# Optimization experiments

Measured on AMD Instinct MI355X. Metric: run time of the kernel, lower is better.

The kernel has to match this reference:

```python
import jax, jax.numpy as jnp
import numpy as np

N = 1024          # number of nodes
E = 32768         # number of edges
S = 4             # num_scales
STEPS = 31        # num_steps
MIN_SIGMA = 0.1
MAX_SIGMA = 3.0
EPS = 1e-12       # F.normalize eps


def setup_inputs() -> dict:
    key = jax.random.key(0)
    k1, k2 = jax.random.split(key, 2)
    coords = jax.random.normal(k1, (N, 3), dtype=jnp.float32)
    edge_index = jax.random.randint(k2, (2, E), 0, N, dtype=jnp.int64)
    # learned parameter, initialized exactly as in the module
    log_sigmas = jnp.linspace(jnp.log(jnp.float32(MIN_SIGMA)),
                              jnp.log(jnp.float32(MAX_SIGMA)), S).astype(jnp.float32)
    return {"coords": coords, "log_sigmas": log_sigmas, "edge_index": edge_index}


def reference(coords, log_sigmas, edge_index):
    n = coords.shape[0]
    # pairwise squared euclidean distances (cdist(..)^2)  [N,N]
    diff = coords[:, None, :] - coords[None, :, :]
    d2 = jnp.sum(diff * diff, axis=-1)

    sigmas = jnp.sort(jnp.exp(log_sigmas))                       # [S]
    w = jnp.exp(-d2[None, :, :] / (2.0 * sigmas[:, None, None] ** 2))  # [S,N,N]
    eye = jnp.eye(n, dtype=w.dtype)
    w = w * (1.0 - eye)                                          # zero diagonal
    row_sum = jnp.sum(w, axis=2, keepdims=True)                  # L1 row norm (w>=0)
    P = w / jnp.maximum(row_sum, EPS)                            # row-stochastic, 0 rows -> 0

    ei, ej = edge_index[0], edge_index[1]

    def step(P_k, _):
        P_k = P_k @ P                                            # batched [S,N,N] GEMM
        diag = jnp.diagonal(P_k, axis1=1, axis2=2)               # [S,N]
        edge = P_k[:, ei, ej]                                    # [S,E]
        return P_k, (diag, edge)

    P0 = jnp.broadcast_to(eye, P.shape)
    _, (diags, edges) = jax.lax.scan(step, P0, None, length=STEPS)
    # diags: [STEPS,S,N] -> node features [N, S*STEPS] (scale-major, step-minor)
    node_features = jnp.transpose(diags, (2, 1, 0)).reshape(n, S * STEPS)
    edge_features = jnp.transpose(edges, (2, 1, 0)).reshape(ei.shape[0], S * STEPS)
    return node_features, edge_features
```

## Files before the change

### kernel.cpp

```cpp
#include <hip/hip_runtime.h>

#define N 1024
#define NE 32768
#define S 4
#define STEPS 31
#define FEAT (S * STEPS)
#define PLANE ((size_t)S * N * N)
#define MAXT 192

typedef short short8 __attribute__((ext_vector_type(8)));
typedef short short4v __attribute__((ext_vector_type(4)));
typedef float f32x4 __attribute__((ext_vector_type(4)));
typedef int int4v __attribute__((ext_vector_type(4)));

__device__ __forceinline__ ushort f2bf(float x) {
    union { float f; unsigned u; } v; v.f = x;
    unsigned r = v.u + 0x7fffu + ((v.u >> 16) & 1u);
    return (ushort)(r >> 16);
}
__device__ __forceinline__ float bf2f(ushort h) {
    union { unsigned u; float f; } v; v.u = ((unsigned)h) << 16;
    return v.f;
}

__device__ __forceinline__ void gload16(const ushort* g, ushort* l) {
    __builtin_amdgcn_global_load_lds(
        (const __attribute__((address_space(1))) unsigned int*)g,
        (__attribute__((address_space(3))) unsigned int*)l, 16, 0, 0);
}

__global__ __launch_bounds__(256) void build_P(const float* __restrict__ coords,
                                               const float* __restrict__ log_sigmas,
                                               ushort* __restrict__ Oh,
                                               ushort* __restrict__ Ol)
{
    const int i   = blockIdx.x;
    const int tid = threadIdx.x;

    float sg[S];
#pragma unroll
    for (int s = 0; s < S; ++s) sg[s] = expf(log_sigmas[s]);
#define CSWP(a, b) { float lo = fminf(sg[a], sg[b]); float hi = fmaxf(sg[a], sg[b]); sg[a] = lo; sg[b] = hi; }
    CSWP(0, 1) CSWP(2, 3) CSWP(0, 2) CSWP(1, 3) CSWP(1, 2)
#undef CSWP
    float inv2s2[S];
#pragma unroll
    for (int s = 0; s < S; ++s) inv2s2[s] = 1.0f / (2.0f * sg[s] * sg[s]);

    const float cx = coords[3 * i + 0];
    const float cy = coords[3 * i + 1];
    const float cz = coords[3 * i + 2];

    float w[4][S];
    float part[S] = {0.f, 0.f, 0.f, 0.f};
#pragma unroll
    for (int c = 0; c < 4; ++c) {
        const int j = tid + c * 256;
        const float dx = cx - coords[3 * j + 0];
        const float dy = cy - coords[3 * j + 1];
        const float dz = cz - coords[3 * j + 2];
        const float d2 = dx * dx + dy * dy + dz * dz;
#pragma unroll
        for (int s = 0; s < S; ++s) {
            const float v = (j == i) ? 0.0f : expf(-d2 * inv2s2[s]);
            w[c][s] = v;
            part[s] += v;
        }
    }

    __shared__ float red[S][256];
#pragma unroll
    for (int s = 0; s < S; ++s) red[s][tid] = part[s];
    __syncthreads();
    for (int st = 128; st > 0; st >>= 1) {
        if (tid < st) {
#pragma unroll
            for (int s = 0; s < S; ++s) red[s][tid] += red[s][tid + st];
        }
        __syncthreads();
    }

    float invden[S];
#pragma unroll
    for (int s = 0; s < S; ++s) invden[s] = 1.0f / fmaxf(red[s][0], 1e-12f);

#pragma unroll
    for (int c = 0; c < 4; ++c) {
        const int j = tid + c * 256;
#pragma unroll
        for (int s = 0; s < S; ++s) {
            const float p = w[c][s] * invden[s];
            const size_t off = ((size_t)s * N + i) * N + j;
            const ushort h = f2bf(p);
            Oh[off] = h;
            Ol[off] = f2bf(p - bf2f(h));
        }
    }
}

__global__ __launch_bounds__(256) void transpose_hl(const ushort* __restrict__ Xh,
                                                    const ushort* __restrict__ Xl,
                                                    ushort* __restrict__ Yh,
                                                    ushort* __restrict__ Yl)
{
    __shared__ float tile[64][65];
    const size_t zb = (size_t)blockIdx.z * N * N;
    const int tr = blockIdx.y * 64, tc = blockIdx.x * 64;
    const int tid = threadIdx.x;
    const int c  = tid & 63;
    const int r0 = tid >> 6;
#pragma unroll
    for (int i = 0; i < 16; ++i) {
        const int r = r0 + i * 4;
        const size_t idx = zb + (size_t)(tr + r) * N + tc + c;
        tile[r][c] = bf2f(Xh[idx]) + bf2f(Xl[idx]);
    }
    __syncthreads();
#pragma unroll
    for (int i = 0; i < 16; ++i) {
        const int r = r0 + i * 4;
        const size_t idx = zb + (size_t)(tc + r) * N + tr + c;
        const float x = tile[c][r];
        const ushort h = f2bf(x);
        Yh[idx] = h;
        if (Yl) Yl[idx] = f2bf(x - bf2f(h));
    }
}

template <bool SPLIT>
__device__ __forceinline__ void gemm_body(const ushort* __restrict__ Ah,
                                          const ushort* __restrict__ Al,
                                          const ushort* __restrict__ BTh,
                                          const ushort* __restrict__ BTl,
                                          ushort* __restrict__ Ch,
                                          ushort* __restrict__ Cl,
                                          ushort* __restrict__ CTh,
                                          ushort* __restrict__ CTl,
                                          int id)
{
    constexpr int NP = SPLIT ? 4 : 2;
    __shared__ ushort smem[4][NP][128 * 32];
    const int tid  = threadIdx.x;
    const int w    = tid >> 6;
    const int lane = tid & 63;
    const int wr   = w >> 1;
    const int wc   = w & 1;

    const int yrow = id & 7;
    const int rest = id >> 3;
    const int xcol = rest & 7;
    const int z    = rest >> 3;
    const size_t zb = (size_t)z * N * N;
    const int tr = yrow * 128;
    const int tc = xcol * 128;

    const ushort* gA0 = Ah  + zb + (size_t)tr * N;
    const ushort* gA1 = SPLIT ? (Al  + zb + (size_t)tr * N) : nullptr;
    const ushort* gB0 = BTh + zb + (size_t)tc * N;
    const ushort* gB1 = SPLIT ? (BTl + zb + (size_t)tc * N) : nullptr;

    f32x4 acc[2][4] = {};

    auto STAGE = [&](int bufi, int k0) __attribute__((always_inline)) {
        const int row = tid >> 2;
        const int kg  = (tid & 3) ^ ((row >> 1) & 3);
        const size_t go = (size_t)row * N + k0 + kg * 8;
        const int lb = w * 512;
        gload16(gA0 + go, &smem[bufi][0][lb]);
        if constexpr (SPLIT) {
            gload16(gA1 + go, &smem[bufi][1][lb]);
            gload16(gB0 + go, &smem[bufi][2][lb]);
            gload16(gB1 + go, &smem[bufi][3][lb]);
        } else {
            gload16(gB0 + go, &smem[bufi][1][lb]);
        }
    };

    const int lrow = lane & 15;
    const int lkg  = lane >> 4;

    auto COMPUTE = [&](int bufi) __attribute__((always_inline)) {
        short8 ah[2], al[2], bh[4], bl[4];
#pragma unroll
        for (int m = 0; m < 2; ++m) {
            const int arow = wr * 32 + m * 16 + lrow;
            const int aoff = arow * 32 + ((lkg ^ ((arow >> 1) & 3)) << 3);
            ah[m] = *(const short8*)&smem[bufi][0][aoff];
            if constexpr (SPLIT) al[m] = *(const short8*)&smem[bufi][1][aoff];
        }
#pragma unroll
        for (int n = 0; n < 4; ++n) {
            const int brow = wc * 64 + n * 16 + lrow;
            const int boff = brow * 32 + ((lkg ^ ((brow >> 1) & 3)) << 3);
            if constexpr (SPLIT) {
                bh[n] = *(const short8*)&smem[bufi][2][boff];
                bl[n] = *(const short8*)&smem[bufi][3][boff];
            } else {
                bh[n] = *(const short8*)&smem[bufi][1][boff];
            }
        }
        __builtin_amdgcn_s_setprio(1);
#pragma unroll
        for (int m = 0; m < 2; ++m)
#pragma unroll
            for (int n = 0; n < 4; ++n) {
                acc[m][n] = __builtin_amdgcn_mfma_f32_16x16x32_bf16(ah[m], bh[n], acc[m][n], 0, 0, 0);
                if constexpr (SPLIT) {
                    acc[m][n] = __builtin_amdgcn_mfma_f32_16x16x32_bf16(ah[m], bl[n], acc[m][n], 0, 0, 0);
                    acc[m][n] = __builtin_amdgcn_mfma_f32_16x16x32_bf16(al[m], bh[n], acc[m][n], 0, 0, 0);
                }
            }
        __builtin_amdgcn_s_setprio(0);
    };

    STAGE(0, 0);
    STAGE(1, 32);
#pragma unroll 1
    for (int t = 0; t < 32; ++t) {
        __builtin_amdgcn_sched_barrier(0);
        if (t < 30) {
            STAGE((t + 2) & 3, (t + 2) * 32);
            if constexpr (SPLIT) asm volatile("s_waitcnt vmcnt(8)" ::: "memory");
            else                 asm volatile("s_waitcnt vmcnt(4)" ::: "memory");
        } else if (t == 30) {
            if constexpr (SPLIT) asm volatile("s_waitcnt vmcnt(4)" ::: "memory");
            else                 asm volatile("s_waitcnt vmcnt(2)" ::: "memory");
        } else {
            asm volatile("s_waitcnt vmcnt(0)" ::: "memory");
        }
        __builtin_amdgcn_s_barrier();
        __builtin_amdgcn_sched_barrier(0);
        COMPUTE(t & 3);
        __builtin_amdgcn_sched_barrier(0);
    }

#pragma unroll
    for (int m = 0; m < 2; ++m)
#pragma unroll
    for (int n = 0; n < 4; ++n) {
        const f32x4 v = acc[m][n];
        ushort hs[4], ls[4];
#pragma unroll
        for (int r = 0; r < 4; ++r) {
            const float x = v[r];
            hs[r] = f2bf(x);
            ls[r] = f2bf(x - bf2f(hs[r]));
        }
        const int row0 = tr + wr * 32 + m * 16 + lkg * 4;
        const int col  = tc + wc * 64 + n * 16 + lrow;
        if (Ch) {
#pragma unroll
            for (int r = 0; r < 4; ++r) {
                const size_t idx = zb + (size_t)(row0 + r) * N + col;
                Ch[idx] = hs[r];
                if (Cl) Cl[idx] = ls[r];
            }
        }
        if (CTh) {
            short4v hv;
            hv[0] = (short)hs[0]; hv[1] = (short)hs[1];
            hv[2] = (short)hs[2]; hv[3] = (short)hs[3];
            *(short4v*)&CTh[zb + (size_t)col * N + row0] = hv;
            if (CTl) {
                short4v lv;
                lv[0] = (short)ls[0]; lv[1] = (short)ls[1];
                lv[2] = (short)ls[2]; lv[3] = (short)ls[3];
                *(short4v*)&CTl[zb + (size_t)col * N + row0] = lv;
            }
        }
    }
}

template <bool SPLIT>
__global__ __launch_bounds__(512) void gemm_tile(const ushort* __restrict__ Ah,
                                                 const ushort* __restrict__ Al,
                                                 const ushort* __restrict__ BTh,
                                                 const ushort* __restrict__ BTl,
                                                 ushort* __restrict__ Ch,
                                                 ushort* __restrict__ Cl,
                                                 ushort* __restrict__ CTh,
                                                 ushort* __restrict__ CTl)
{
    gemm_body<SPLIT>(Ah, Al, BTh, BTl, Ch, Cl, CTh, CTl, blockIdx.x);
}

__global__ __launch_bounds__(512) void gemm_leaf(
    const ushort* A0, const ushort* B0, ushort* C0, ushort* T0,
    const ushort* A1, const ushort* B1, ushort* C1, ushort* T1,
    const ushort* A2, const ushort* B2, ushort* C2, ushort* T2,
    const ushort* A3, const ushort* B3, ushort* C3, ushort* T3,
    const ushort* A4, const ushort* B4, ushort* C4, ushort* T4)
{
    const int op = blockIdx.x >> 8;
    const int id = blockIdx.x & 255;
    const ushort* A; const ushort* B; ushort* C; ushort* T;
    if      (op == 0) { A = A0; B = B0; C = C0; T = T0; }
    else if (op == 1) { A = A1; B = B1; C = C1; T = T1; }
    else if (op == 2) { A = A2; B = B2; C = C2; T = T2; }
    else if (op == 3) { A = A3; B = B3; C = C3; T = T3; }
    else              { A = A4; B = B4; C = C4; T = T4; }
    gemm_body<false>(A, nullptr, B, nullptr, C, nullptr, T, nullptr, id);
}

__global__ __launch_bounds__(128) void quant8(const ushort* __restrict__ X12,
                                              const ushort* __restrict__ X24,
                                              unsigned char* __restrict__ Q,
                                              float* __restrict__ sc)
{
    const int id  = blockIdx.x;
    const int pl  = id >> 12;
    const int row = id & 4095;
    const int tid = threadIdx.x;
    const ushort* src = (pl ? X24 : X12) + (size_t)row * N;
    unsigned char* dst = Q + (size_t)pl * PLANE + (size_t)row * N;

    float v[8];
    const short8 x = ((const short8*)src)[tid];
    float mx = 0.0f;
#pragma unroll
    for (int e = 0; e < 8; ++e) { v[e] = bf2f((ushort)x[e]); mx = fmaxf(mx, v[e]); }
#pragma unroll
    for (int d = 1; d < 64; d <<= 1) mx = fmaxf(mx, __shfl_xor(mx, d, 64));
    __shared__ float wmx[2];
    if ((tid & 63) == 0) wmx[tid >> 6] = mx;
    __syncthreads();
    mx = fmaxf(fmaxf(wmx[0], wmx[1]), 1e-30f);

    const float inv = 127.0f / mx;
    uint2 q;
    q.x = 0; q.y = 0;
#pragma unroll
    for (int e = 0; e < 4; ++e) {
        q.x |= ((unsigned)(int)(v[e] * inv + 0.5f)) << (e * 8);
        q.y |= ((unsigned)(int)(v[4 + e] * inv + 0.5f)) << (e * 8);
    }
    ((uint2*)dst)[tid] = q;
    if (tid == 0) sc[id] = mx * (1.0f / 127.0f);
}

__global__ __launch_bounds__(256) void gather_hl(const ushort* __restrict__ Ph,
                                                 const ushort* __restrict__ Pl,
                                                 const int* __restrict__ eidx,
                                                 float* __restrict__ out,
                                                 int t)
{
    const int tid = blockIdx.x * blockDim.x + threadIdx.x;
    const int ND = S * N;
    if (tid < ND) {
        const int s = tid >> 10;
        const int n = tid & (N - 1);
        const size_t off = ((size_t)s * N + n) * N + n;
        float v = bf2f(Ph[off]);
        if (Pl) v += bf2f(Pl[off]);
        out[(size_t)n * FEAT + s * STEPS + t] = v;
    } else {
        const int idx = tid - ND;
        if (idx >= S * NE) return;
        const int s = idx >> 15;
        const int e = idx & (NE - 1);
        const int i = eidx[e];
        const int j = eidx[NE + e];
        const size_t off = ((size_t)s * N + i) * N + j;
        float v = bf2f(Ph[off]);
        if (Pl) v += bf2f(Pl[off]);
        out[(size_t)N * FEAT + (size_t)e * FEAT + s * STEPS + t] = v;
    }
}

__global__ __launch_bounds__(256) void zero_aux(int* __restrict__ p, int n)
{
    for (int i = blockIdx.x * 256 + threadIdx.x; i < n; i += gridDim.x * 256) p[i] = 0;
}

__global__ __launch_bounds__(256) void edge_hist(const int* __restrict__ eidx,
                                                 int* __restrict__ hist)
{
    const int e = blockIdx.x * 256 + threadIdx.x;
    if (e < NE) atomicAdd(&hist[eidx[NE + e]], 1);
}

__global__ __launch_bounds__(1024) void scan1024(const int* __restrict__ hist,
                                                 int* __restrict__ offs)
{
    __shared__ int tmp[1024];
    const int t = threadIdx.x;
    tmp[t] = hist[t];
    __syncthreads();
    for (int d = 1; d < 1024; d <<= 1) {
        int v = (t >= d) ? tmp[t - d] : 0;
        __syncthreads();
        tmp[t] += v;
        __syncthreads();
    }
    offs[t + 1] = tmp[t];
    if (t == 0) offs[0] = 0;
}

__global__ __launch_bounds__(256) void edge_scatter(const int* __restrict__ eidx,
                                                    const int* __restrict__ offs,
                                                    int* __restrict__ cursor,
                                                    int* __restrict__ perm)
{
    const int e = blockIdx.x * 256 + threadIdx.x;
    if (e < NE) {
        const int j = eidx[NE + e];
        const int pos = atomicAdd(&cursor[j], 1);
        perm[offs[j] + pos] = e;
    }
}

__global__ __launch_bounds__(256) void extract_k(const ushort* __restrict__ BT18,
                                                 const ushort* __restrict__ bt9p,
                                                 const ushort* __restrict__ bt10p,
                                                 const ushort* __restrict__ bt11p,
                                                 const ushort* __restrict__ bt12p,
                                                 const unsigned char* __restrict__ Q,
                                                 const float* __restrict__ sc,
                                                 const int* __restrict__ eidx,
                                                 const int* __restrict__ perm,
                                                 const int* __restrict__ offs,
                                                 float* __restrict__ out)
{
    const int id = blockIdx.x;
    const int s  = (id & 7) >> 1;
    const int j  = (id >> 3) * 2 + (id & 1);
    const int tid  = threadIdx.x;
    const int wave = tid >> 6;
    const int lane = tid & 63;

    __shared__ __align__(16) ushort bt[12][1032];
    __shared__ __align__(16) unsigned char btq[12][1040];
    __shared__ int tlist[MAXT];
    __shared__ int elist[MAXT];
    __shared__ float saA[MAXT], saC[MAXT];
    __shared__ int   rowmaxi[12];
    __shared__ float sbq[12], sbinv[12];

    if (tid < 12) rowmaxi[tid] = 0;
    __syncthreads();

    const int base  = offs[j];
    const int cnt   = min(offs[j + 1] - base, MAXT - 1);
    const int ntask = cnt + 1;
    const int ngrp  = (ntask + 15) >> 4;

    for (int t0 = tid; t0 < MAXT; t0 += 256) {
        int e = -2, i = j;
        if (t0 < cnt)       { e = perm[base + t0]; i = eidx[e]; }
        else if (t0 == cnt) { e = -1; }
        tlist[t0] = i;
        elist[t0] = e;
    }

    const size_t rowbase = ((size_t)s * N + j) * N;
    for (int c = tid; c < 12 * 128; c += 256) {
        const int b  = c >> 7;
        const int ch = c & 127;
        const ushort* q = (b < 8) ? (BT18 + (size_t)b * PLANE)
                        : (b == 8 ? bt9p : b == 9 ? bt10p : b == 10 ? bt11p : bt12p);
        const short8 v = *(const short8*)&q[rowbase + ch * 8];
        *(short8*)&bt[b][ch * 8] = v;
        float mx = 0.0f;
#pragma unroll
        for (int x = 0; x < 8; ++x) mx = fmaxf(mx, bf2f((ushort)v[x]));
        atomicMax(&rowmaxi[b], __float_as_int(mx));
    }
    __syncthreads();

    if (tid < 12) {
        const float rm = fmaxf(__int_as_float(rowmaxi[tid]), 1e-30f);
        sbq[tid]   = rm * (1.0f / 127.0f);
        sbinv[tid] = 127.0f / rm;
    }
    __syncthreads();

    for (int c = tid; c < 12 * 128; c += 256) {
        const int b  = c >> 7;
        const int ch = c & 127;
        const float inv = sbinv[b];
        uint2 q; q.x = 0; q.y = 0;
#pragma unroll
        for (int x = 0; x < 4; ++x) {
            q.x |= ((unsigned)(int)(bf2f(bt[b][ch * 8 + x]) * inv + 0.5f)) << (x * 8);
            q.y |= ((unsigned)(int)(bf2f(bt[b][ch * 8 + 4 + x]) * inv + 0.5f)) << (x * 8);
        }
        *(uint2*)&btq[b][ch * 8] = q;
    }
    for (int t0 = tid; t0 < MAXT; t0 += 256) {
        const int i = tlist[t0];
        saA[t0] = sc[s * N + i];
        saC[t0] = sc[S * N + s * N + i];
    }
    for (int t0 = tid; t0 < ntask; t0 += 256) {
        const int i = tlist[t0];
        const int e = elist[t0];
        const size_t obase = (e >= 0)
            ? ((size_t)N * FEAT + (size_t)e * FEAT + (size_t)s * STEPS)
            : ((size_t)j * FEAT + (size_t)s * STEPS);
#pragma unroll
        for (int b = 0; b < 12; ++b)
            out[obase + b] = bf2f(bt[b][i]);
    }
    __syncthreads();

    const int nidx = lane & 15;
    const int koff = (lane >> 4) * 16;
    const unsigned char* btq_ptr = &btq[nidx < 12 ? nidx : 0][koff];

    for (int g = wave; g < ngrp; g += 4) {
        const int i = tlist[g * 16 + nidx];
        const size_t abase = ((size_t)s * N + i) * N + koff;
        const unsigned char* pa0 = Q + abase;
        const unsigned char* pa1 = Q + PLANE + abase;

        int4v acc0 = {}, acc1 = {};
#pragma unroll 8
        for (int ks = 0; ks < 16; ++ks) {
            const int4v bv  = *(const int4v*)(btq_ptr + ks * 64);
            const int4v av0 = *(const int4v*)(pa0 + ks * 64);
            const int4v av1 = *(const int4v*)(pa1 + ks * 64);
            acc0 = __builtin_amdgcn_mfma_i32_16x16x64_i8(av0, bv, acc0, 0, 0, 0);
            acc1 = __builtin_amdgcn_mfma_i32_16x16x64_i8(av1, bv, acc1, 0, 0, 0);
        }

        if (nidx < 12) {
            const int m0 = (lane >> 4) * 4;
            const float sb = sbq[nidx];
#pragma unroll
            for (int r = 0; r < 4; ++r) {
                const int task = g * 16 + m0 + r;
                const int e = elist[task];
                if (e >= -1) {
                    const size_t obase = (e >= 0)
                        ? ((size_t)N * FEAT + (size_t)e * FEAT + (size_t)s * STEPS)
                        : ((size_t)j * FEAT + (size_t)s * STEPS);
                    out[obase + 12 + nidx] = (float)acc0[r] * saA[task] * sb;
                    if (nidx < 7)
                        out[obase + 24 + nidx] = (float)acc1[r] * saC[task] * sb;
                }
            }
        }
    }
}

extern "C" void kernel_launch(void* const* d_in, const int* in_sizes, int n_in,
                              void* d_out, int out_size, void* d_ws, size_t ws_size,
                              hipStream_t stream)
{
    const float* coords     = (const float*)d_in[0];
    const float* log_sigmas = (const float*)d_in[1];
    const int*   eidx       = (const int*)d_in[2];
    float*       out        = (float*)d_out;

    ushort* W = (ushort*)d_ws;
    const dim3 tgrid(16, 16, S);
    ushort* const NUL = nullptr;
#define PS(k) (W + (size_t)(k) * PLANE)

    const size_t AUX_INTS = 1024 + 1024 + 1025 + NE + 2 * S * N;
    const size_t NEED_A   = 15 * PLANE * sizeof(ushort) + AUX_INTS * sizeof(int);

    if (ws_size >= NEED_A) {
        int* hist   = (int*)(W + 15 * PLANE);
        int* cursor = hist + 1024;
        int* offs   = cursor + 1024;
        int* perm   = offs + 1025;
        float* sc   = (float*)(perm + NE);

        zero_aux<<<8, 256, 0, stream>>>(hist, 2048);
        edge_hist<<<NE / 256, 256, 0, stream>>>(eidx, hist);
        scan1024<<<1, 1024, 0, stream>>>(hist, offs);
        edge_scatter<<<NE / 256, 256, 0, stream>>>(eidx, offs, cursor, perm);

        build_P<<<N, 256, 0, stream>>>(coords, log_sigmas, PS(12), PS(13));
        transpose_hl<<<tgrid, 256, 0, stream>>>(PS(12), PS(13), PS(0), PS(8));

        gemm_tile<true><<<256, 512, 0, stream>>>(PS(12), PS(13), PS(0), PS(8),
                                                 PS(9), PS(10), PS(1), PS(11));
        gemm_tile<true><<<256, 512, 0, stream>>>(PS(9), PS(10), PS(1), PS(11),
                                                 PS(12), PS(13), PS(3), PS(14));
        gemm_leaf<<<768, 512, 0, stream>>>(
            PS(9), PS(0), NUL, PS(2),
            PS(12), PS(0), NUL, PS(4),
            PS(12), PS(1), NUL, PS(5),
            NUL, NUL, NUL, NUL,
            NUL, NUL, NUL, NUL);
        gemm_tile<true><<<256, 512, 0, stream>>>(PS(12), PS(13), PS(3), PS(14),
                                                 PS(9), NUL, PS(7), NUL);
        gemm_leaf<<<1280, 512, 0, stream>>>(
            PS(12), PS(2), NUL, PS(6),
            PS(9), PS(0), NUL, PS(10),
            PS(9), PS(1), NUL, PS(11),
            PS(9), PS(2), NUL, PS(13),
            PS(9), PS(3), PS(14), PS(8));
        gemm_tile<false><<<256, 512, 0, stream>>>(PS(14), NUL, PS(8), NUL,
                                                  PS(12), NUL, NUL, NUL);
        quant8<<<2 * S * N, 128, 0, stream>>>(PS(14), PS(12),
                                              (unsigned char*)PS(9), sc);

        extract_k<<<N * S, 256, 0, stream>>>(W, PS(10), PS(11), PS(13), PS(8),
                                             (const unsigned char*)PS(9), sc,
                                             eidx, perm, offs, out);
    } else {
        ushort* ping_h = PS(0); ushort* ping_l = PS(1);
        ushort* pong_h = PS(2); ushort* pong_l = PS(3);
        ushort* bt_h   = PS(4); ushort* bt_l   = PS(5);
        const int gather_blocks = (S * N + S * NE + 255) / 256;

        build_P<<<N, 256, 0, stream>>>(coords, log_sigmas, ping_h, ping_l);
        gather_hl<<<gather_blocks, 256, 0, stream>>>(ping_h, ping_l, eidx, out, 0);
        transpose_hl<<<tgrid, 256, 0, stream>>>(ping_h, ping_l, bt_h, bt_l);

        ushort* cur_h = ping_h; ushort* cur_l = ping_l;
        ushort* nxt_h = pong_h; ushort* nxt_l = pong_l;
        for (int k = 2; k <= STEPS; ++k) {
            gemm_tile<true><<<256, 512, 0, stream>>>(cur_h, cur_l, bt_h, bt_l,
                                                     nxt_h, nxt_l, NUL, NUL);
            gather_hl<<<gather_blocks, 256, 0, stream>>>(nxt_h, nxt_l, eidx, out, k - 1);
            ushort* th = cur_h; ushort* tl = cur_l;
            cur_h = nxt_h; cur_l = nxt_l; nxt_h = th; nxt_l = tl;
        }
    }
#undef PS
}
```

Baseline: 328.3 us.

## Reduce stored power planes to 8 and compute more steps via int8 MFMA extraction

Changes the power-decomposition plan so that only P^1..P^8 are materialized as transposed bf16 planes, with three int8-quantized base planes (P^8, P^16, P^24) used in extract_k. Steps 9-31 for each edge are now computed as dot products against the 8 cached rows. This replaces two extra leaf GEMMs, and part of the fifth op, with a third int8 MFMA accumulator in the extraction kernel. It trades dense GEMM work for more per-edge int8 dot products and an extra quantized plane, which adds quantization error for more of the steps.

```diff
diff --git a/kernel.cpp b/kernel.cpp
--- a/kernel.cpp
+++ b/kernel.cpp
@@ -287,23 +287,20 @@
 __global__ __launch_bounds__(512) void gemm_leaf(
     const ushort* A0, const ushort* B0, ushort* C0, ushort* T0,
     const ushort* A1, const ushort* B1, ushort* C1, ushort* T1,
-    const ushort* A2, const ushort* B2, ushort* C2, ushort* T2,
-    const ushort* A3, const ushort* B3, ushort* C3, ushort* T3,
-    const ushort* A4, const ushort* B4, ushort* C4, ushort* T4)
+    const ushort* A2, const ushort* B2, ushort* C2, ushort* T2)
 {
     const int op = blockIdx.x >> 8;
     const int id = blockIdx.x & 255;
     const ushort* A; const ushort* B; ushort* C; ushort* T;
     if      (op == 0) { A = A0; B = B0; C = C0; T = T0; }
     else if (op == 1) { A = A1; B = B1; C = C1; T = T1; }
-    else if (op == 2) { A = A2; B = B2; C = C2; T = T2; }
-    else if (op == 3) { A = A3; B = B3; C = C3; T = T3; }
-    else              { A = A4; B = B4; C = C4; T = T4; }
+    else              { A = A2; B = B2; C = C2; T = T2; }
     gemm_body<false>(A, nullptr, B, nullptr, C, nullptr, T, nullptr, id);
 }
 
-__global__ __launch_bounds__(128) void quant8(const ushort* __restrict__ X12,
-                                              const ushort* __restrict__ X24,
+__global__ __launch_bounds__(128) void quant8(const ushort* __restrict__ X0,
+                                              const ushort* __restrict__ X1,
+                                              const ushort* __restrict__ X2,
                                               unsigned char* __restrict__ Q,
                                               float* __restrict__ sc)
 {
@@ -311,7 +308,7 @@
     const int pl  = id >> 12;
     const int row = id & 4095;
     const int tid = threadIdx.x;
-    const ushort* src = (pl ? X24 : X12) + (size_t)row * N;
+    const ushort* src = (pl == 0 ? X0 : pl == 1 ? X1 : X2) + (size_t)row * N;
     unsigned char* dst = Q + (size_t)pl * PLANE + (size_t)row * N;
 
     float v[8];
@@ -410,10 +407,6 @@
 }
 
 __global__ __launch_bounds__(256) void extract_k(const ushort* __restrict__ BT18,
-                                                 const ushort* __restrict__ bt9p,
-                                                 const ushort* __restrict__ bt10p,
-                                                 const ushort* __restrict__ bt11p,
-                                                 const ushort* __restrict__ bt12p,
                                                  const unsigned char* __restrict__ Q,
                                                  const float* __restrict__ sc,
                                                  const int* __restrict__ eidx,
@@ -428,15 +421,15 @@
     const int wave = tid >> 6;
     const int lane = tid & 63;
 
-    __shared__ __align__(16) ushort bt[12][1032];
-    __shared__ __align__(16) unsigned char btq[12][1040];
+    __shared__ __align__(16) ushort bt[8][1032];
+    __shared__ __align__(16) unsigned char btq[8][1040];
     __shared__ int tlist[MAXT];
     __shared__ int elist[MAXT];
-    __shared__ float saA[MAXT], saC[MAXT];
-    __shared__ int   rowmaxi[12];
-    __shared__ float sbq[12], sbinv[12];
-
-    if (tid < 12) rowmaxi[tid] = 0;
+    __shared__ float saA[MAXT], saB[MAXT], saC[MAXT];
+    __shared__ int   rowmaxi[8];
+    __shared__ float sbq[8], sbinv[8];
+
+    if (tid < 8) rowmaxi[tid] = 0;
     __syncthreads();
 
     const int base  = offs[j];
@@ -453,12 +446,10 @@
     }
 
     const size_t rowbase = ((size_t)s * N + j) * N;
-    for (int c = tid; c < 12 * 128; c += 256) {
+    for (int c = tid; c < 8 * 128; c += 256) {
         const int b  = c >> 7;
         const int ch = c & 127;
-        const ushort* q = (b < 8) ? (BT18 + (size_t)b * PLANE)
-                        : (b == 8 ? bt9p : b == 9 ? bt10p : b == 10 ? bt11p : bt12p);
-        const short8 v = *(const short8*)&q[rowbase + ch * 8];
+        const short8 v = *(const short8*)&BT18[(size_t)b * PLANE + rowbase + ch * 8];
         *(short8*)&bt[b][ch * 8] = v;
         float mx = 0.0f;
 #pragma unroll
@@ -467,14 +458,14 @@
     }
     __syncthreads();
 
-    if (tid < 12) {
+    if (tid < 8) {
         const float rm = fmaxf(__int_as_float(rowmaxi[tid]), 1e-30f);
         sbq[tid]   = rm * (1.0f / 127.0f);
         sbinv[tid] = 127.0f / rm;
     }
     __syncthreads();
 
-    for (int c = tid; c < 12 * 128; c += 256) {
+    for (int c = tid; c < 8 * 128; c += 256) {
         const int b  = c >> 7;
         const int ch = c & 127;
         const float inv = sbinv[b];
@@ -488,8 +479,9 @@
     }
     for (int t0 = tid; t0 < MAXT; t0 += 256) {
         const int i = tlist[t0];
-        saA[t0] = sc[s * N + i];
-        saC[t0] = sc[S * N + s * N + i];
+        saA[t0] = sc[0 * S * N + s * N + i];
+        saB[t0] = sc[1 * S * N + s * N + i];
+        saC[t0] = sc[2 * S * N + s * N + i];
     }
     for (int t0 = tid; t0 < ntask; t0 += 256) {
         const int i = tlist[t0];
@@ -498,32 +490,35 @@
             ? ((size_t)N * FEAT + (size_t)e * FEAT + (size_t)s * STEPS)
             : ((size_t)j * FEAT + (size_t)s * STEPS);
 #pragma unroll
-        for (int b = 0; b < 12; ++b)
+        for (int b = 0; b < 8; ++b)
             out[obase + b] = bf2f(bt[b][i]);
     }
     __syncthreads();
 
     const int nidx = lane & 15;
     const int koff = (lane >> 4) * 16;
-    const unsigned char* btq_ptr = &btq[nidx < 12 ? nidx : 0][koff];
+    const unsigned char* btq_ptr = &btq[nidx & 7][koff];
 
     for (int g = wave; g < ngrp; g += 4) {
         const int i = tlist[g * 16 + nidx];
         const size_t abase = ((size_t)s * N + i) * N + koff;
         const unsigned char* pa0 = Q + abase;
         const unsigned char* pa1 = Q + PLANE + abase;
-
-        int4v acc0 = {}, acc1 = {};
-#pragma unroll 8
+        const unsigned char* pa2 = Q + 2 * PLANE + abase;
+
+        int4v acc0 = {}, acc1 = {}, acc2 = {};
+#pragma unroll 4
         for (int ks = 0; ks < 16; ++ks) {
             const int4v bv  = *(const int4v*)(btq_ptr + ks * 64);
             const int4v av0 = *(const int4v*)(pa0 + ks * 64);
             const int4v av1 = *(const int4v*)(pa1 + ks * 64);
+            const int4v av2 = *(const int4v*)(pa2 + ks * 64);
             acc0 = __builtin_amdgcn_mfma_i32_16x16x64_i8(av0, bv, acc0, 0, 0, 0);
             acc1 = __builtin_amdgcn_mfma_i32_16x16x64_i8(av1, bv, acc1, 0, 0, 0);
-        }
-
-        if (nidx < 12) {
+            acc2 = __builtin_amdgcn_mfma_i32_16x16x64_i8(av2, bv, acc2, 0, 0, 0);
+        }
+
+        if (nidx < 8) {
             const int m0 = (lane >> 4) * 4;
             const float sb = sbq[nidx];
 #pragma unroll
@@ -534,9 +529,10 @@
                     const size_t obase = (e >= 0)
                         ? ((size_t)N * FEAT + (size_t)e * FEAT + (size_t)s * STEPS)
                         : ((size_t)j * FEAT + (size_t)s * STEPS);
-                    out[obase + 12 + nidx] = (float)acc0[r] * saA[task] * sb;
+                    out[obase + 8  + nidx] = (float)acc0[r] * saA[task] * sb;
+                    out[obase + 16 + nidx] = (float)acc1[r] * saB[task] * sb;
                     if (nidx < 7)
-                        out[obase + 24 + nidx] = (float)acc1[r] * saC[task] * sb;
+                        out[obase + 24 + nidx] = (float)acc2[r] * saC[task] * sb;
                 }
             }
         }
@@ -557,7 +553,7 @@
     ushort* const NUL = nullptr;
 #define PS(k) (W + (size_t)(k) * PLANE)
 
-    const size_t AUX_INTS = 1024 + 1024 + 1025 + NE + 2 * S * N;
+    const size_t AUX_INTS = 1024 + 1024 + 1025 + NE + 3 * S * N;
     const size_t NEED_A   = 15 * PLANE * sizeof(ushort) + AUX_INTS * sizeof(int);
 
     if (ws_size >= NEED_A) {
@@ -567,40 +563,35 @@
         int* perm   = offs + 1025;
         float* sc   = (float*)(perm + NE);
 
+        unsigned char* Q = (unsigned char*)PS(8);
+
         zero_aux<<<8, 256, 0, stream>>>(hist, 2048);
         edge_hist<<<NE / 256, 256, 0, stream>>>(eidx, hist);
         scan1024<<<1, 1024, 0, stream>>>(hist, offs);
         edge_scatter<<<NE / 256, 256, 0, stream>>>(eidx, offs, cursor, perm);
 
-        build_P<<<N, 256, 0, stream>>>(coords, log_sigmas, PS(12), PS(13));
-        transpose_hl<<<tgrid, 256, 0, stream>>>(PS(12), PS(13), PS(0), PS(8));
-
-        gemm_tile<true><<<256, 512, 0, stream>>>(PS(12), PS(13), PS(0), PS(8),
-                                                 PS(9), PS(10), PS(1), PS(11));
-        gemm_tile<true><<<256, 512, 0, stream>>>(PS(9), PS(10), PS(1), PS(11),
-                                                 PS(12), PS(13), PS(3), PS(14));
+        build_P<<<N, 256, 0, stream>>>(coords, log_sigmas, PS(10), PS(11));
+        transpose_hl<<<tgrid, 256, 0, stream>>>(PS(10), PS(11), PS(0), PS(12));
+
+        gemm_tile<true><<<256, 512, 0, stream>>>(PS(10), PS(11), PS(0), PS(12),
+                                                 PS(13), PS(14), PS(1), PS(9));
+        gemm_tile<true><<<256, 512, 0, stream>>>(PS(13), PS(14), PS(1), PS(9),
+                                                 PS(10), PS(11), PS(3), PS(12));
         gemm_leaf<<<768, 512, 0, stream>>>(
-            PS(9), PS(0), NUL, PS(2),
-            PS(12), PS(0), NUL, PS(4),
-            PS(12), PS(1), NUL, PS(5),
-            NUL, NUL, NUL, NUL,
+            PS(13), PS(0), NUL, PS(2),
+            PS(10), PS(0), NUL, PS(4),
+            PS(10), PS(1), NUL, PS(5));
+        gemm_tile<true><<<256, 512, 0, stream>>>(PS(10), PS(11), PS(3), PS(12),
+                                                 PS(13), NUL, PS(7), NUL);
+        gemm_leaf<<<512, 512, 0, stream>>>(
+            PS(10), PS(2), NUL, PS(6),
+            PS(13), PS(7), PS(14), NUL,
             NUL, NUL, NUL, NUL);
-        gemm_tile<true><<<256, 512, 0, stream>>>(PS(12), PS(13), PS(3), PS(14),
-                                                 PS(9), NUL, PS(7), NUL);
-        gemm_leaf<<<1280, 512, 0, stream>>>(
-            PS(12), PS(2), NUL, PS(6),
-            PS(9), PS(0), NUL, PS(10),
-            PS(9), PS(1), NUL, PS(11),
-            PS(9), PS(2), NUL, PS(13),
-            PS(9), PS(3), PS(14), PS(8));
-        gemm_tile<false><<<256, 512, 0, stream>>>(PS(14), NUL, PS(8), NUL,
-                                                  PS(12), NUL, NUL, NUL);
-        quant8<<<2 * S * N, 128, 0, stream>>>(PS(14), PS(12),
-                                              (unsigned char*)PS(9), sc);
-
-        extract_k<<<N * S, 256, 0, stream>>>(W, PS(10), PS(11), PS(13), PS(8),
-                                             (const unsigned char*)PS(9), sc,
-                                             eidx, perm, offs, out);
+        gemm_tile<false><<<256, 512, 0, stream>>>(PS(14), NUL, PS(7), NUL,
+                                                  PS(10), NUL, NUL, NUL);
+        quant8<<<3 * S * N, 128, 0, stream>>>(PS(13), PS(14), PS(10), Q, sc);
+
+        extract_k<<<N * S, 256, 0, stream>>>(W, Q, sc, eidx, perm, offs, out);
     } else {
         ushort* ping_h = PS(0); ushort* ping_l = PS(1);
         ushort* pong_h = PS(2); ushort* pong_l = PS(3);
```

Measured after the change: 301.1 us. 1.09x faster.
